# Performance work log

Hardware: AMD Instinct MI355X
Metric: run time of the kernel (lower is better)

Reference implementation:

```python
import jax, jax.numpy as jnp
import numpy as np

IN_FEATURES = 8192
OUT_FEATURES = 8192
MAX_STATES = 100
THRESHOLD = MAX_STATES // 2  # 50


def setup_inputs() -> dict:
    key = jax.random.key(0)
    k1, k2 = jax.random.split(key)
    spike_input = jax.random.uniform(k1, (IN_FEATURES,), dtype=jnp.float32)
    # buffer init: randn(out, in) * 2.0 + threshold - 1.0
    synapse_states = (jax.random.normal(k2, (OUT_FEATURES, IN_FEATURES), dtype=jnp.float32)
                      * 2.0 + float(THRESHOLD) - 1.0)
    membrane_potential = jnp.zeros((OUT_FEATURES,), dtype=jnp.float32)
    adaptive_threshold = jnp.full((OUT_FEATURES,), 2.5, dtype=jnp.float32)
    eligibility_trace = jnp.zeros((OUT_FEATURES, IN_FEATURES), dtype=jnp.float32)
    return {
        'spike_input': spike_input,
        'synapse_states': synapse_states,
        'membrane_potential': membrane_potential,
        'adaptive_threshold': adaptive_threshold,
        'eligibility_trace': eligibility_trace,
    }


def reference(spike_input, synapse_states, membrane_potential, adaptive_threshold, eligibility_trace):
    # ternary (here effectively binary) weights via threshold compare
    w = (synapse_states > float(THRESHOLD)).astype(jnp.float32)  # [O, I]
    x = spike_input.reshape(-1)                                   # [I] (batch must be 1)
    current = w @ x                                               # [O]
    # LIF membrane update: v <- 0.8*v + I
    v_mem = membrane_potential * 0.8 + current
    spikes = (v_mem >= adaptive_threshold).astype(jnp.float32)    # [O]
    # eligibility trace: decay + outer-product potentiation, clamp to [0, 10]
    new_trace = jnp.clip(eligibility_trace * 0.7 + jnp.outer(spikes, x) * 3.0, 0.0, 10.0)
    # adaptive threshold homeostasis, clamp to [0.5, 10]
    new_threshold = jnp.clip(adaptive_threshold + (spikes - 0.05) * 0.1, 0.5, 10.0)
    # soft reset: v <- v * (1 - spike) * 0.2
    new_v_mem = v_mem * (1.0 - spikes) * 0.2
    return spikes, new_v_mem, new_trace, new_threshold
```

## Files before the change

### kernel.cpp

```cpp
#include <hip/hip_runtime.h>

#define IN_F 8192
#define OUT_F 8192
#define BLOCK 256

__global__ __launch_bounds__(BLOCK) void snn_fused_kernel(
    const float* __restrict__ x,
    const float* __restrict__ syn,
    const float* __restrict__ mp,
    const float* __restrict__ at,
    const float* __restrict__ trace,
    float* __restrict__ spikes_out,
    float* __restrict__ vmem_out,
    float* __restrict__ trace_out,
    float* __restrict__ thr_out)
{
    const int o   = blockIdx.x;
    const int tid = threadIdx.x;
    const int n4  = IN_F / 4;

    const float4* __restrict__ syn4 = reinterpret_cast<const float4*>(syn + (size_t)o * IN_F);
    const float4* __restrict__ x4   = reinterpret_cast<const float4*>(x);

    float partial = 0.0f;
    #pragma unroll 4
    for (int i = tid; i < n4; i += BLOCK) {
        float4 s  = syn4[i];
        float4 xv = x4[i];
        partial += (s.x > 50.0f ? xv.x : 0.0f);
        partial += (s.y > 50.0f ? xv.y : 0.0f);
        partial += (s.z > 50.0f ? xv.z : 0.0f);
        partial += (s.w > 50.0f ? xv.w : 0.0f);
    }

    #pragma unroll
    for (int off = 32; off > 0; off >>= 1)
        partial += __shfl_down(partial, off, 64);

    __shared__ float wsum[BLOCK / 64];
    __shared__ float s_spike;
    if ((tid & 63) == 0) wsum[tid >> 6] = partial;
    __syncthreads();

    if (tid == 0) {
        float cur = wsum[0] + wsum[1] + wsum[2] + wsum[3];
        float v   = mp[o] * 0.8f + cur;
        float a   = at[o];
        float sp  = (v >= a) ? 1.0f : 0.0f;
        spikes_out[o] = sp;
        vmem_out[o]   = v * (1.0f - sp) * 0.2f;
        float nt = a + (sp - 0.05f) * 0.1f;
        thr_out[o] = fminf(fmaxf(nt, 0.5f), 10.0f);
        s_spike = sp;
    }
    __syncthreads();

    const float sp3 = s_spike * 3.0f;
    const float4* __restrict__ tr4  = reinterpret_cast<const float4*>(trace + (size_t)o * IN_F);
    float4* __restrict__       out4 = reinterpret_cast<float4*>(trace_out + (size_t)o * IN_F);

    #pragma unroll 4
    for (int i = tid; i < n4; i += BLOCK) {
        float4 t  = tr4[i];
        float4 xv = x4[i];
        float4 r;
        r.x = fminf(fmaxf(t.x * 0.7f + sp3 * xv.x, 0.0f), 10.0f);
        r.y = fminf(fmaxf(t.y * 0.7f + sp3 * xv.y, 0.0f), 10.0f);
        r.z = fminf(fmaxf(t.z * 0.7f + sp3 * xv.z, 0.0f), 10.0f);
        r.w = fminf(fmaxf(t.w * 0.7f + sp3 * xv.w, 0.0f), 10.0f);
        out4[i] = r;
    }
}

extern "C" void kernel_launch(void* const* d_in, const int* in_sizes, int n_in,
                              void* d_out, int out_size, void* d_ws, size_t ws_size,
                              hipStream_t stream) {
    const float* x     = (const float*)d_in[0];
    const float* syn   = (const float*)d_in[1];
    const float* mp    = (const float*)d_in[2];
    const float* at    = (const float*)d_in[3];
    const float* trace = (const float*)d_in[4];

    float* out        = (float*)d_out;
    float* spikes_out = out;
    float* vmem_out   = out + OUT_F;
    float* trace_out  = out + 2 * (size_t)OUT_F;
    float* thr_out    = out + 2 * (size_t)OUT_F + (size_t)OUT_F * IN_F;

    snn_fused_kernel<<<OUT_F, BLOCK, 0, stream>>>(
        x, syn, mp, at, trace, spikes_out, vmem_out, trace_out, thr_out);
}
```

Before: 148.2 us.

## Assign one wavefront per output row and use nontemporal trace stores

```diff
diff --git a/kernel.cpp b/kernel.cpp
--- a/kernel.cpp
+++ b/kernel.cpp
@@ -3,6 +3,10 @@
 #define IN_F 8192
 #define OUT_F 8192
 #define BLOCK 256
+#define WAVES_PER_BLOCK (BLOCK / 64)
+#define N4 (IN_F / 4)
+
+typedef float v4f __attribute__((ext_vector_type(4)));
 
 __global__ __launch_bounds__(BLOCK) void snn_fused_kernel(
     const float* __restrict__ x,
@@ -15,18 +19,18 @@
     float* __restrict__ trace_out,
     float* __restrict__ thr_out)
 {
-    const int o   = blockIdx.x;
-    const int tid = threadIdx.x;
-    const int n4  = IN_F / 4;
+    const int wave = threadIdx.x >> 6;
+    const int lane = threadIdx.x & 63;
+    const int o    = blockIdx.x * WAVES_PER_BLOCK + wave;
 
-    const float4* __restrict__ syn4 = reinterpret_cast<const float4*>(syn + (size_t)o * IN_F);
-    const float4* __restrict__ x4   = reinterpret_cast<const float4*>(x);
+    const v4f* __restrict__ syn4 = reinterpret_cast<const v4f*>(syn + (size_t)o * IN_F);
+    const v4f* __restrict__ x4   = reinterpret_cast<const v4f*>(x);
 
     float partial = 0.0f;
-    #pragma unroll 4
-    for (int i = tid; i < n4; i += BLOCK) {
-        float4 s  = syn4[i];
-        float4 xv = x4[i];
+    #pragma unroll 8
+    for (int i = lane; i < N4; i += 64) {
+        v4f s  = syn4[i];
+        v4f xv = x4[i];
         partial += (s.x > 50.0f ? xv.x : 0.0f);
         partial += (s.y > 50.0f ? xv.y : 0.0f);
         partial += (s.z > 50.0f ? xv.z : 0.0f);
@@ -36,39 +40,31 @@
     #pragma unroll
     for (int off = 32; off > 0; off >>= 1)
         partial += __shfl_down(partial, off, 64);
+    const float cur = __shfl(partial, 0, 64);
 
-    __shared__ float wsum[BLOCK / 64];
-    __shared__ float s_spike;
-    if ((tid & 63) == 0) wsum[tid >> 6] = partial;
-    __syncthreads();
-
-    if (tid == 0) {
-        float cur = wsum[0] + wsum[1] + wsum[2] + wsum[3];
-        float v   = mp[o] * 0.8f + cur;
-        float a   = at[o];
-        float sp  = (v >= a) ? 1.0f : 0.0f;
+    const float v  = mp[o] * 0.8f + cur;
+    const float a  = at[o];
+    const float sp = (v >= a) ? 1.0f : 0.0f;
+    if (lane == 0) {
         spikes_out[o] = sp;
         vmem_out[o]   = v * (1.0f - sp) * 0.2f;
-        float nt = a + (sp - 0.05f) * 0.1f;
-        thr_out[o] = fminf(fmaxf(nt, 0.5f), 10.0f);
-        s_spike = sp;
+        thr_out[o]    = fminf(fmaxf(a + (sp - 0.05f) * 0.1f, 0.5f), 10.0f);
     }
-    __syncthreads();
 
-    const float sp3 = s_spike * 3.0f;
-    const float4* __restrict__ tr4  = reinterpret_cast<const float4*>(trace + (size_t)o * IN_F);
-    float4* __restrict__       out4 = reinterpret_cast<float4*>(trace_out + (size_t)o * IN_F);
+    const float sp3 = sp * 3.0f;
+    const v4f* __restrict__ tr4 = reinterpret_cast<const v4f*>(trace + (size_t)o * IN_F);
+    v4f*       out4             = reinterpret_cast<v4f*>(trace_out + (size_t)o * IN_F);
 
-    #pragma unroll 4
-    for (int i = tid; i < n4; i += BLOCK) {
-        float4 t  = tr4[i];
-        float4 xv = x4[i];
-        float4 r;
+    #pragma unroll 8
+    for (int i = lane; i < N4; i += 64) {
+        v4f t  = tr4[i];
+        v4f xv = x4[i];
+        v4f r;
         r.x = fminf(fmaxf(t.x * 0.7f + sp3 * xv.x, 0.0f), 10.0f);
         r.y = fminf(fmaxf(t.y * 0.7f + sp3 * xv.y, 0.0f), 10.0f);
         r.z = fminf(fmaxf(t.z * 0.7f + sp3 * xv.z, 0.0f), 10.0f);
         r.w = fminf(fmaxf(t.w * 0.7f + sp3 * xv.w, 0.0f), 10.0f);
-        out4[i] = r;
+        __builtin_nontemporal_store(r, &out4[i]);
     }
 }
 
@@ -87,6 +83,6 @@
     float* trace_out  = out + 2 * (size_t)OUT_F;
     float* thr_out    = out + 2 * (size_t)OUT_F + (size_t)OUT_F * IN_F;
 
-    snn_fused_kernel<<<OUT_F, BLOCK, 0, stream>>>(
+    snn_fused_kernel<<<OUT_F / WAVES_PER_BLOCK, BLOCK, 0, stream>>>(
         x, syn, mp, at, trace, spikes_out, vmem_out, trace_out, thr_out);
 }
```

Result: slower. 157.1 us (+6.0%).
